# Kernel tuning notes

Measured on AMD Instinct MI355X. Metric: run time of the kernel, lower is better.

Reference implementation:

```python
import jax, jax.numpy as jnp
import numpy as np

HEAD_DIM = 64  # scale = head_dim ** -0.5


def setup_inputs() -> dict:
    key = jax.random.key(0)
    ks = jax.random.split(key, 5)
    B, S, E = 8, 8192, 1024
    L, D = 64, 256          # n_latent_vec, latent_dim
    H = HEAD_DIM
    return {
        "input_tensor": jax.random.normal(ks[0], (B, S, E), dtype=jnp.float32),
        "latents": jax.random.normal(ks[1], (L, D), dtype=jnp.float32),
        "Wq": jax.random.normal(ks[2], (H, D), dtype=jnp.float32) * (1.0 / np.sqrt(D)),
        "Wk": jax.random.normal(ks[3], (H, E), dtype=jnp.float32) * (1.0 / np.sqrt(E)),
        "Wv": jax.random.normal(ks[4], (H, E), dtype=jnp.float32) * (1.0 / np.sqrt(E)),
    }


def reference(input_tensor, latents, Wq, Wk, Wv):
    # non-cached path, seq_len == max_seq_len so no truncation
    # queries: broadcast shared latents over batch -> [B, L, H]
    q = jnp.einsum('ld,hd->lh', latents, Wq)                 # [L, H]
    k = jnp.einsum('bse,he->bsh', input_tensor, Wk)           # [B, S, H]
    v = jnp.einsum('bse,he->bsh', input_tensor, Wv)           # [B, S, H]
    scale = HEAD_DIM ** -0.5
    scores = jnp.einsum('lh,bsh->bls', q, k) * scale          # [B, L, S]
    weights = jax.nn.softmax(scores, axis=-1)                 # dropout is identity (p=0 / eval)
    out = jnp.einsum('bls,bsh->blh', weights, v)              # [B, L, H]
    return out
```

## Files before the change

### kernel.cpp

```cpp
#include <hip/hip_runtime.h>
#include <stdint.h>


typedef __attribute__((__ext_vector_type__(4))) float f32x4;
typedef __attribute__((__ext_vector_type__(8))) short bf16x8;

__device__ __forceinline__ unsigned short f2bf(float f) {
    union { float f; uint32_t u; } v; v.f = f;
    uint32_t u = v.u;
    return (unsigned short)((u + 0x7fffu + ((u >> 16) & 1u)) >> 16);
}

__global__ __launch_bounds__(256) void prep_kernel(
    const float* __restrict__ latents, const float* __restrict__ Wq,
    const float* __restrict__ Wk, const float* __restrict__ Wv,
    unsigned short* __restrict__ wkv, unsigned short* __restrict__ qbf)
{
    const int blk = blockIdx.x, tid = threadIdx.x;
    if (blk < 128) {
        const float* src = (blk < 64) ? (Wk + (size_t)blk * 1024)
                                      : (Wv + (size_t)(blk - 64) * 1024);
        for (int i = tid; i < 1024; i += 256)
            wkv[(size_t)blk * 1024 + i] = f2bf(src[i]);
    } else {
        const int l = (blk - 128) * 4 + (tid >> 6);
        const int h = tid & 63;
        float a = 0.f;
        for (int d = 0; d < 256; ++d)
            a += latents[l * 256 + d] * Wq[h * 256 + d];
        qbf[l * 64 + h] = f2bf(a * 0.125f);
    }
}

__global__ __launch_bounds__(256) void proj_kernel(
    const float* __restrict__ x, const unsigned short* __restrict__ wkv,
    unsigned short* __restrict__ kv)
{
    __shared__ unsigned short smem[20480];
    unsigned short* Ab = smem;
    unsigned short* Bb = smem + 10240;

    const int tid = threadIdx.x;
    const size_t r0 = (size_t)blockIdx.x * 128;
    const int wave = tid >> 6, lane = tid & 63;
    const int g = lane >> 4, c = lane & 15;
    const int wr = wave >> 1, wc = wave & 1;

    const int rowA = tid >> 3, colA = (tid & 7) * 4;
    const int rowB = tid >> 2, colB = (tid & 3) * 8;

    f32x4 acc[4][4];
    #pragma unroll
    for (int i = 0; i < 4; ++i)
        #pragma unroll
        for (int j = 0; j < 4; ++j)
            acc[i][j] = f32x4{0.f, 0.f, 0.f, 0.f};

    f32x4 areg[4];
    uint4  breg[2];

    #pragma unroll
    for (int i = 0; i < 4; ++i)
        areg[i] = *(const f32x4*)(x + (r0 + rowA + 32 * i) * 1024 + colA);
    #pragma unroll
    for (int j = 0; j < 2; ++j)
        breg[j] = *(const uint4*)(wkv + (size_t)(rowB + 64 * j) * 1024 + colB);
    #pragma unroll
    for (int i = 0; i < 4; ++i) {
        unsigned long long pk =
            (unsigned long long)f2bf(areg[i][0])        |
            ((unsigned long long)f2bf(areg[i][1]) << 16) |
            ((unsigned long long)f2bf(areg[i][2]) << 32) |
            ((unsigned long long)f2bf(areg[i][3]) << 48);
        *(unsigned long long*)&Ab[(rowA + 32 * i) * 40 + colA] = pk;
    }
    #pragma unroll
    for (int j = 0; j < 2; ++j)
        *(uint4*)&Bb[(rowB + 64 * j) * 40 + colB] = breg[j];
    __syncthreads();

    for (int t = 0; t < 32; ++t) {
        const int buf = t & 1;
        if (t < 31) {
            const int e0 = (t + 1) * 32;
            #pragma unroll
            for (int i = 0; i < 4; ++i)
                areg[i] = *(const f32x4*)(x + (r0 + rowA + 32 * i) * 1024 + e0 + colA);
            #pragma unroll
            for (int j = 0; j < 2; ++j)
                breg[j] = *(const uint4*)(wkv + (size_t)(rowB + 64 * j) * 1024 + e0 + colB);
        }
        bf16x8 af[4], bfr[4];
        #pragma unroll
        for (int ml = 0; ml < 4; ++ml)
            af[ml] = *(const bf16x8*)&Ab[(buf * 128 + 64 * wr + 16 * ml + c) * 40 + 8 * g];
        #pragma unroll
        for (int nc = 0; nc < 4; ++nc)
            bfr[nc] = *(const bf16x8*)&Bb[(buf * 128 + 64 * wc + 16 * nc + c) * 40 + 8 * g];
        #pragma unroll
        for (int ml = 0; ml < 4; ++ml)
            #pragma unroll
            for (int nc = 0; nc < 4; ++nc)
                acc[ml][nc] = __builtin_amdgcn_mfma_f32_16x16x32_bf16(
                    af[ml], bfr[nc], acc[ml][nc], 0, 0, 0);
        if (t < 31) {
            const int nb = buf ^ 1;
            #pragma unroll
            for (int i = 0; i < 4; ++i) {
                unsigned long long pk =
                    (unsigned long long)f2bf(areg[i][0])        |
                    ((unsigned long long)f2bf(areg[i][1]) << 16) |
                    ((unsigned long long)f2bf(areg[i][2]) << 32) |
                    ((unsigned long long)f2bf(areg[i][3]) << 48);
                *(unsigned long long*)&Ab[(nb * 128 + rowA + 32 * i) * 40 + colA] = pk;
            }
            #pragma unroll
            for (int j = 0; j < 2; ++j)
                *(uint4*)&Bb[(nb * 128 + rowB + 64 * j) * 40 + colB] = breg[j];
        }
        __syncthreads();
    }

    unsigned short* Cs = smem;
    #pragma unroll
    for (int ml = 0; ml < 4; ++ml)
        #pragma unroll
        for (int nc = 0; nc < 4; ++nc)
            #pragma unroll
            for (int r = 0; r < 4; ++r)
                Cs[(64 * wr + 16 * ml + 4 * g + r) * 136 + 64 * wc + 16 * nc + c] =
                    f2bf(acc[ml][nc][r]);
    __syncthreads();
    const int rowO = tid >> 4, colO = (tid & 15) * 8;
    #pragma unroll
    for (int i = 0; i < 8; ++i) {
        const int row = rowO + 16 * i;
        uint4 vv = *(const uint4*)&Cs[row * 136 + colO];
        *(uint4*)(kv + (r0 + row) * 128 + colO) = vv;
    }
}

__global__ __launch_bounds__(256) void attn_kernel(
    const unsigned short* __restrict__ kv, const unsigned short* __restrict__ qbf,
    float* __restrict__ Opart, float* __restrict__ mpart, float* __restrict__ spart)
{
    __shared__ unsigned short kvs[128][136];
    __shared__ unsigned short qs[64][72];
    __shared__ unsigned short Ps[64][136];
    __shared__ float red[4][64];
    __shared__ float Mrow[64];

    const int tid = threadIdx.x, wave = tid >> 6, lane = tid & 63;
    const int g = lane >> 4, c = lane & 15;
    const int b = blockIdx.x >> 6, ch = blockIdx.x & 63;
    const size_t base = (size_t)b * 8192 + (size_t)ch * 128;

    {
        const int rowK = tid >> 4, colK = (tid & 15) * 8;
        #pragma unroll
        for (int i = 0; i < 8; ++i) {
            const int row = rowK + 16 * i;
            *(uint4*)&kvs[row][colK] = *(const uint4*)(kv + (base + row) * 128 + colK);
        }
        const int rowQ = tid >> 3, colQ = (tid & 7) * 8;
        #pragma unroll
        for (int i = 0; i < 2; ++i) {
            const int row = rowQ + 32 * i;
            *(uint4*)&qs[row][colQ] = *(const uint4*)(qbf + row * 64 + colQ);
        }
    }
    __syncthreads();

    f32x4 sc[4][2];
    #pragma unroll
    for (int ml = 0; ml < 4; ++ml)
        #pragma unroll
        for (int ns = 0; ns < 2; ++ns)
            sc[ml][ns] = f32x4{0.f, 0.f, 0.f, 0.f};
    #pragma unroll
    for (int k0 = 0; k0 < 2; ++k0) {
        bf16x8 aq[4];
        #pragma unroll
        for (int ml = 0; ml < 4; ++ml)
            aq[ml] = *(const bf16x8*)&qs[16 * ml + c][32 * k0 + 8 * g];
        #pragma unroll
        for (int ns = 0; ns < 2; ++ns) {
            bf16x8 bk = *(const bf16x8*)&kvs[32 * wave + 16 * ns + c][32 * k0 + 8 * g];
            #pragma unroll
            for (int ml = 0; ml < 4; ++ml)
                sc[ml][ns] = __builtin_amdgcn_mfma_f32_16x16x32_bf16(
                    aq[ml], bk, sc[ml][ns], 0, 0, 0);
        }
    }

    float mloc[4][4];
    #pragma unroll
    for (int ml = 0; ml < 4; ++ml)
        #pragma unroll
        for (int r = 0; r < 4; ++r)
            mloc[ml][r] = fmaxf(sc[ml][0][r], sc[ml][1][r]);
    #pragma unroll
    for (int off = 1; off <= 8; off <<= 1)
        #pragma unroll
        for (int ml = 0; ml < 4; ++ml)
            #pragma unroll
            for (int r = 0; r < 4; ++r)
                mloc[ml][r] = fmaxf(mloc[ml][r], __shfl_xor(mloc[ml][r], off));
    if (c == 0)
        #pragma unroll
        for (int ml = 0; ml < 4; ++ml)
            #pragma unroll
            for (int r = 0; r < 4; ++r)
                red[wave][16 * ml + 4 * g + r] = mloc[ml][r];
    __syncthreads();
    if (tid < 64) {
        float m = red[0][tid];
        m = fmaxf(m, red[1][tid]); m = fmaxf(m, red[2][tid]); m = fmaxf(m, red[3][tid]);
        Mrow[tid] = m;
    }
    __syncthreads();

    float ssum[4][4];
    #pragma unroll
    for (int ml = 0; ml < 4; ++ml)
        #pragma unroll
        for (int r = 0; r < 4; ++r)
            ssum[ml][r] = 0.f;
    #pragma unroll
    for (int ml = 0; ml < 4; ++ml)
        #pragma unroll
        for (int r = 0; r < 4; ++r) {
            const int l = 16 * ml + 4 * g + r;
            const float mr = Mrow[l];
            #pragma unroll
            for (int ns = 0; ns < 2; ++ns) {
                float p = __expf(sc[ml][ns][r] - mr);
                unsigned short pb = f2bf(p);
                Ps[l][32 * wave + 16 * ns + c] = pb;
                union { uint32_t u; float f; } pv; pv.u = (uint32_t)pb << 16;
                ssum[ml][r] += pv.f;
            }
        }
    #pragma unroll
    for (int off = 1; off <= 8; off <<= 1)
        #pragma unroll
        for (int ml = 0; ml < 4; ++ml)
            #pragma unroll
            for (int r = 0; r < 4; ++r)
                ssum[ml][r] += __shfl_xor(ssum[ml][r], off);
    if (c == 0)
        #pragma unroll
        for (int ml = 0; ml < 4; ++ml)
            #pragma unroll
            for (int r = 0; r < 4; ++r)
                red[wave][16 * ml + 4 * g + r] = ssum[ml][r];
    __syncthreads();
    if (tid < 64) {
        const float s = red[0][tid] + red[1][tid] + red[2][tid] + red[3][tid];
        mpart[(size_t)blockIdx.x * 64 + tid] = Mrow[tid];
        spart[(size_t)blockIdx.x * 64 + tid] = s;
    }

    f32x4 o[4];
    #pragma unroll
    for (int nh = 0; nh < 4; ++nh) o[nh] = f32x4{0.f, 0.f, 0.f, 0.f};
    #pragma unroll
    for (int ks = 0; ks < 4; ++ks) {
        bf16x8 ap = *(const bf16x8*)&Ps[16 * wave + c][32 * ks + 8 * g];
        #pragma unroll
        for (int nh = 0; nh < 4; ++nh) {
            bf16x8 bv;
            #pragma unroll
            for (int j = 0; j < 8; ++j)
                bv[j] = (short)kvs[32 * ks + 8 * g + j][64 + 16 * nh + c];
            o[nh] = __builtin_amdgcn_mfma_f32_16x16x32_bf16(ap, bv, o[nh], 0, 0, 0);
        }
    }
    const size_t pb = (size_t)blockIdx.x * 64;
    #pragma unroll
    for (int nh = 0; nh < 4; ++nh)
        #pragma unroll
        for (int r = 0; r < 4; ++r) {
            const int l = 16 * wave + 4 * g + r;
            const int h = 16 * nh + c;
            Opart[(pb + l) * 64 + h] = o[nh][r];
        }
}

__global__ __launch_bounds__(64) void combine_kernel(
    const float* __restrict__ Opart, const float* __restrict__ mpart,
    const float* __restrict__ spart, float* __restrict__ out)
{
    const int b = blockIdx.x >> 6, l = blockIdx.x & 63, h = threadIdx.x;
    float M = -3.0e38f;
    for (int ch = 0; ch < 64; ++ch)
        M = fmaxf(M, mpart[((size_t)(b * 64 + ch)) * 64 + l]);
    float den = 0.f, acc = 0.f;
    for (int ch = 0; ch < 64; ++ch) {
        const size_t idx = ((size_t)(b * 64 + ch)) * 64 + l;
        const float w = __expf(mpart[idx] - M);
        den += w * spart[idx];
        acc += w * Opart[idx * 64 + h];
    }
    out[((size_t)blockIdx.x) * 64 + h] = acc / den;
}

extern "C" void kernel_launch(void* const* d_in, const int* in_sizes, int n_in,
                              void* d_out, int out_size, void* d_ws, size_t ws_size,
                              hipStream_t stream)
{
    const float* x       = (const float*)d_in[0];
    const float* latents = (const float*)d_in[1];
    const float* Wq      = (const float*)d_in[2];
    const float* Wk      = (const float*)d_in[3];
    const float* Wv      = (const float*)d_in[4];
    float* out = (float*)d_out;
    char* ws = (char*)d_ws;

    unsigned short* wkv = (unsigned short*)(ws);
    unsigned short* qbf = (unsigned short*)(ws + 262144);
    unsigned short* kvb = (unsigned short*)(ws + 270336);
    float* Opart = (float*)(ws + 270336 + 16777216);
    float* mpart = (float*)(ws + 270336 + 16777216 + 8388608);
    float* spart = (float*)(ws + 270336 + 16777216 + 8388608 + 131072);

    hipLaunchKernelGGL(prep_kernel, dim3(144), dim3(256), 0, stream,
                       latents, Wq, Wk, Wv, wkv, qbf);
    hipLaunchKernelGGL(proj_kernel, dim3(512), dim3(256), 0, stream, x, wkv, kvb);
    hipLaunchKernelGGL(attn_kernel, dim3(512), dim3(256), 0, stream,
                       kvb, qbf, Opart, mpart, spart);
    hipLaunchKernelGGL(combine_kernel, dim3(512), dim3(64), 0, stream,
                       Opart, mpart, spart, out);
}
```

Baseline: 97.48 us.

## Fuse K/V projection into attention kernel, keeping KV tile in shared memory

Merges the projection and attention kernels so each block computes its 128-row K/V tile and immediately runs the partial attention on it from LDS. This removes the bf16 KV round trip through global memory (16 MB write plus read) and one kernel launch. Shared memory per block grows to roughly 68 KB, which may reduce occupancy. The combine kernel loops also get unroll pragmas.

```diff
diff --git a/kernel.cpp b/kernel.cpp
--- a/kernel.cpp
+++ b/kernel.cpp
@@ -32,19 +32,34 @@
     }
 }
 
-__global__ __launch_bounds__(256) void proj_kernel(
+__global__ __launch_bounds__(256) void fused_kernel(
     const float* __restrict__ x, const unsigned short* __restrict__ wkv,
-    unsigned short* __restrict__ kv)
+    const unsigned short* __restrict__ qbf,
+    float* __restrict__ Opart, float* __restrict__ mpart, float* __restrict__ spart)
 {
-    __shared__ unsigned short smem[20480];
+    __shared__ unsigned short smem[33792];
     unsigned short* Ab = smem;
     unsigned short* Bb = smem + 10240;
+    unsigned short* Cs = smem;
+    unsigned short* qs = smem + 20480;
+    unsigned short* Ps = smem + 25088;
+    __shared__ float red[4][64];
+    __shared__ float Mrow[64];
 
     const int tid = threadIdx.x;
-    const size_t r0 = (size_t)blockIdx.x * 128;
     const int wave = tid >> 6, lane = tid & 63;
     const int g = lane >> 4, c = lane & 15;
     const int wr = wave >> 1, wc = wave & 1;
+    const size_t r0 = (size_t)blockIdx.x * 128;
+
+    {
+        const int rowQ = tid >> 3, colQ = (tid & 7) * 8;
+        #pragma unroll
+        for (int i = 0; i < 2; ++i) {
+            const int row = rowQ + 32 * i;
+            *(uint4*)&qs[row * 72 + colQ] = *(const uint4*)(qbf + row * 64 + colQ);
+        }
+    }
 
     const int rowA = tid >> 3, colA = (tid & 7) * 4;
     const int rowB = tid >> 2, colB = (tid & 3) * 8;
@@ -121,7 +136,6 @@
         __syncthreads();
     }
 
-    unsigned short* Cs = smem;
     #pragma unroll
     for (int ml = 0; ml < 4; ++ml)
         #pragma unroll
@@ -131,45 +145,6 @@
                 Cs[(64 * wr + 16 * ml + 4 * g + r) * 136 + 64 * wc + 16 * nc + c] =
                     f2bf(acc[ml][nc][r]);
     __syncthreads();
-    const int rowO = tid >> 4, colO = (tid & 15) * 8;
-    #pragma unroll
-    for (int i = 0; i < 8; ++i) {
-        const int row = rowO + 16 * i;
-        uint4 vv = *(const uint4*)&Cs[row * 136 + colO];
-        *(uint4*)(kv + (r0 + row) * 128 + colO) = vv;
-    }
-}
-
-__global__ __launch_bounds__(256) void attn_kernel(
-    const unsigned short* __restrict__ kv, const unsigned short* __restrict__ qbf,
-    float* __restrict__ Opart, float* __restrict__ mpart, float* __restrict__ spart)
-{
-    __shared__ unsigned short kvs[128][136];
-    __shared__ unsigned short qs[64][72];
-    __shared__ unsigned short Ps[64][136];
-    __shared__ float red[4][64];
-    __shared__ float Mrow[64];
-
-    const int tid = threadIdx.x, wave = tid >> 6, lane = tid & 63;
-    const int g = lane >> 4, c = lane & 15;
-    const int b = blockIdx.x >> 6, ch = blockIdx.x & 63;
-    const size_t base = (size_t)b * 8192 + (size_t)ch * 128;
-
-    {
-        const int rowK = tid >> 4, colK = (tid & 15) * 8;
-        #pragma unroll
-        for (int i = 0; i < 8; ++i) {
-            const int row = rowK + 16 * i;
-            *(uint4*)&kvs[row][colK] = *(const uint4*)(kv + (base + row) * 128 + colK);
-        }
-        const int rowQ = tid >> 3, colQ = (tid & 7) * 8;
-        #pragma unroll
-        for (int i = 0; i < 2; ++i) {
-            const int row = rowQ + 32 * i;
-            *(uint4*)&qs[row][colQ] = *(const uint4*)(qbf + row * 64 + colQ);
-        }
-    }
-    __syncthreads();
 
     f32x4 sc[4][2];
     #pragma unroll
@@ -182,10 +157,10 @@
         bf16x8 aq[4];
         #pragma unroll
         for (int ml = 0; ml < 4; ++ml)
-            aq[ml] = *(const bf16x8*)&qs[16 * ml + c][32 * k0 + 8 * g];
+            aq[ml] = *(const bf16x8*)&qs[(16 * ml + c) * 72 + 32 * k0 + 8 * g];
         #pragma unroll
         for (int ns = 0; ns < 2; ++ns) {
-            bf16x8 bk = *(const bf16x8*)&kvs[32 * wave + 16 * ns + c][32 * k0 + 8 * g];
+            bf16x8 bk = *(const bf16x8*)&Cs[(32 * wave + 16 * ns + c) * 136 + 32 * k0 + 8 * g];
             #pragma unroll
             for (int ml = 0; ml < 4; ++ml)
                 sc[ml][ns] = __builtin_amdgcn_mfma_f32_16x16x32_bf16(
@@ -236,7 +211,7 @@
             for (int ns = 0; ns < 2; ++ns) {
                 float p = __expf(sc[ml][ns][r] - mr);
                 unsigned short pb = f2bf(p);
-                Ps[l][32 * wave + 16 * ns + c] = pb;
+                Ps[l * 136 + 32 * wave + 16 * ns + c] = pb;
                 union { uint32_t u; float f; } pv; pv.u = (uint32_t)pb << 16;
                 ssum[ml][r] += pv.f;
             }
@@ -266,13 +241,13 @@
     for (int nh = 0; nh < 4; ++nh) o[nh] = f32x4{0.f, 0.f, 0.f, 0.f};
     #pragma unroll
     for (int ks = 0; ks < 4; ++ks) {
-        bf16x8 ap = *(const bf16x8*)&Ps[16 * wave + c][32 * ks + 8 * g];
+        bf16x8 ap = *(const bf16x8*)&Ps[(16 * wave + c) * 136 + 32 * ks + 8 * g];
         #pragma unroll
         for (int nh = 0; nh < 4; ++nh) {
             bf16x8 bv;
             #pragma unroll
             for (int j = 0; j < 8; ++j)
-                bv[j] = (short)kvs[32 * ks + 8 * g + j][64 + 16 * nh + c];
+                bv[j] = (short)Cs[(32 * ks + 8 * g + j) * 136 + 64 + 16 * nh + c];
             o[nh] = __builtin_amdgcn_mfma_f32_16x16x32_bf16(ap, bv, o[nh], 0, 0, 0);
         }
     }
@@ -293,9 +268,11 @@
 {
     const int b = blockIdx.x >> 6, l = blockIdx.x & 63, h = threadIdx.x;
     float M = -3.0e38f;
+    #pragma unroll 8
     for (int ch = 0; ch < 64; ++ch)
         M = fmaxf(M, mpart[((size_t)(b * 64 + ch)) * 64 + l]);
     float den = 0.f, acc = 0.f;
+    #pragma unroll 8
     for (int ch = 0; ch < 64; ++ch) {
         const size_t idx = ((size_t)(b * 64 + ch)) * 64 + l;
         const float w = __expf(mpart[idx] - M);
@@ -319,16 +296,14 @@
 
     unsigned short* wkv = (unsigned short*)(ws);
     unsigned short* qbf = (unsigned short*)(ws + 262144);
-    unsigned short* kvb = (unsigned short*)(ws + 270336);
-    float* Opart = (float*)(ws + 270336 + 16777216);
-    float* mpart = (float*)(ws + 270336 + 16777216 + 8388608);
-    float* spart = (float*)(ws + 270336 + 16777216 + 8388608 + 131072);
+    float* Opart = (float*)(ws + 270336);
+    float* mpart = (float*)(ws + 270336 + 8388608);
+    float* spart = (float*)(ws + 270336 + 8388608 + 131072);
 
     hipLaunchKernelGGL(prep_kernel, dim3(144), dim3(256), 0, stream,
                        latents, Wq, Wk, Wv, wkv, qbf);
-    hipLaunchKernelGGL(proj_kernel, dim3(512), dim3(256), 0, stream, x, wkv, kvb);
-    hipLaunchKernelGGL(attn_kernel, dim3(512), dim3(256), 0, stream,
-                       kvb, qbf, Opart, mpart, spart);
+    hipLaunchKernelGGL(fused_kernel, dim3(512), dim3(256), 0, stream,
+                       x, wkv, qbf, Opart, mpart, spart);
     hipLaunchKernelGGL(combine_kernel, dim3(512), dim3(64), 0, stream,
                        Opart, mpart, spart, out);
 }
```

New measurement: 81.75 us. 16.1% less time.
